# Performance work log

Measured on AMD Instinct MI355X. Metric: run time of the kernel, lower is better.

## Reference

```python
import jax, jax.numpy as jnp
import numpy as np

B, IN_F, K_INT, OUT_F = 256, 512, 75, 64
INIT = 0.05


def setup_inputs() -> dict:
    key = jax.random.key(0)
    k_x, k_t = jax.random.split(key)
    x = jax.random.normal(k_x, (B, IN_F), dtype=jnp.float32)
    T = jax.random.normal(k_t, (IN_F, K_INT, OUT_F), dtype=jnp.float32) * INIT
    return {"x": x, "T": T}


def reference(x, T):
    # M: [B, K, O] = x @ T flattened over (K, O)
    Bn = x.shape[0]
    M = (x @ T.reshape(T.shape[0], -1)).reshape(Bn, T.shape[1], T.shape[2])
    # pairwise L1 distance over K: [B, B, O]
    # (original materializes [B, B, K, O] broadcasted diff; same math)
    M_diff = M[None, :, :, :] - M[:, None, :, :]
    distance = jnp.abs(M_diff).sum(axis=2)           # [B, B, O]
    exp_distance = jnp.exp(-distance)                # [B, B, O]
    minibatch_features = exp_distance.sum(axis=1) - 1.0  # [B, O]; -1 removes self-distance
    return minibatch_features
```

## Files before the change

kernel.cpp:

```cpp
#include <hip/hip_runtime.h>


typedef __attribute__((ext_vector_type(8))) short bf16x8;
typedef __attribute__((ext_vector_type(4))) float f32x4;
typedef unsigned short u16;
typedef unsigned int u32;

__device__ inline u16 f2bf(float f) {
  u32 u = __float_as_uint(f);
  return (u16)((u + 0x7FFFu + ((u >> 16) & 1u)) >> 16);
}
__device__ inline short bftrunc(float f) {
  return (short)(__float_as_uint(f) >> 16);
}
__device__ inline float bflo(u32 u) { return __uint_as_float(u << 16); }
__device__ inline float bfhi(u32 u) { return __uint_as_float(u & 0xFFFF0000u); }

__global__ __launch_bounds__(256) void md_gemm_direct(const float* __restrict__ x,
                                                      const float* __restrict__ T,
                                                      float* __restrict__ Mt2) {
  const int tid = threadIdx.x;
  const int l = tid & 63, w = tid >> 6;
  const int bx = blockIdx.x;
  const int b0 = (blockIdx.y << 6) + ((w & 1) << 5);
  const int z = blockIdx.z;
  const int lr = l & 15;
  const int ko = (l >> 4) << 3;
  const int oh = (w >> 1) << 5;

  const float* At = T + (z * 256 + ko) * 4800 + bx * 64 + oh + lr;
  const float* Bx0 = x + (b0 + lr) * 512 + z * 256 + ko;
  const float* Bx1 = Bx0 + 16 * 512;

  f32x4 d00 = {0.f, 0.f, 0.f, 0.f}, d01 = d00, d10 = d00, d11 = d00;

#pragma unroll 2
  for (int kk = 0; kk < 8; ++kk) {
    bf16x8 a0, a1, f0, f1;
    const float* Ak = At + (kk << 5) * 4800;
#pragma unroll
    for (int e = 0; e < 8; ++e) {
      a0[e] = bftrunc(Ak[e * 4800]);
      a1[e] = bftrunc(Ak[e * 4800 + 16]);
    }
    const float4 b00 = *reinterpret_cast<const float4*>(Bx0 + (kk << 5));
    const float4 b01 = *reinterpret_cast<const float4*>(Bx0 + (kk << 5) + 4);
    const float4 b10 = *reinterpret_cast<const float4*>(Bx1 + (kk << 5));
    const float4 b11 = *reinterpret_cast<const float4*>(Bx1 + (kk << 5) + 4);
    f0[0] = bftrunc(b00.x); f0[1] = bftrunc(b00.y); f0[2] = bftrunc(b00.z); f0[3] = bftrunc(b00.w);
    f0[4] = bftrunc(b01.x); f0[5] = bftrunc(b01.y); f0[6] = bftrunc(b01.z); f0[7] = bftrunc(b01.w);
    f1[0] = bftrunc(b10.x); f1[1] = bftrunc(b10.y); f1[2] = bftrunc(b10.z); f1[3] = bftrunc(b10.w);
    f1[4] = bftrunc(b11.x); f1[5] = bftrunc(b11.y); f1[6] = bftrunc(b11.z); f1[7] = bftrunc(b11.w);

    d00 = __builtin_amdgcn_mfma_f32_16x16x32_bf16(a0, f0, d00, 0, 0, 0);
    d01 = __builtin_amdgcn_mfma_f32_16x16x32_bf16(a0, f1, d01, 0, 0, 0);
    d10 = __builtin_amdgcn_mfma_f32_16x16x32_bf16(a1, f0, d10, 0, 0, 0);
    d11 = __builtin_amdgcn_mfma_f32_16x16x32_bf16(a1, f1, d11, 0, 0, 0);
  }

  float* Mt = Mt2 + z * 1228800;
  const int n0 = (bx << 6) + oh;
#pragma unroll
  for (int r = 0; r < 4; ++r) {
    const int row = ((l >> 4) << 2) + r;
    {
      const int n = n0 + row;
      float* base = Mt + (n & 63) * 19200 + (n >> 6) * 256;
      base[b0 + lr] = d00[r];
      base[b0 + 16 + lr] = d01[r];
    }
    {
      const int n = n0 + 16 + row;
      float* base = Mt + (n & 63) * 19200 + (n >> 6) * 256;
      base[b0 + lr] = d10[r];
      base[b0 + 16 + lr] = d11[r];
    }
  }
}

#define PSTR 72
__global__ __launch_bounds__(256) void md_pair_sym(const float* __restrict__ Mt2,
                                                   float* __restrict__ out) {
  const int bid = blockIdx.x;
  const int o = bid & 63;
  const int tp = bid >> 6;
  const int TI[10] = {0, 0, 0, 0, 1, 1, 1, 2, 2, 3};
  const int TJ[10] = {0, 1, 2, 3, 1, 2, 3, 2, 3, 3};
  const int ti = TI[tp], tj = TJ[tp];
  const bool diag = (ti == tj);
  const int tid = threadIdx.x;

  __shared__ alignas(16) u16 panel[2][75 * PSTR];
  u16* Mi = panel[0];
  u16* Mj = diag ? panel[0] : panel[1];

  const float* M0 = Mt2 + o * 19200;
  const float* M1 = M0 + 1228800;

  for (int idx = tid; idx < 1200; idx += 256) {
    const int kk = idx >> 4, q = idx & 15;
    {
      const int goff = kk * 256 + (ti << 6) + (q << 2);
      const float4 v0 = *reinterpret_cast<const float4*>(M0 + goff);
      const float4 v1 = *reinterpret_cast<const float4*>(M1 + goff);
      uint2 p;
      p.x = (u32)f2bf(v0.x + v1.x) | ((u32)f2bf(v0.y + v1.y) << 16);
      p.y = (u32)f2bf(v0.z + v1.z) | ((u32)f2bf(v0.w + v1.w) << 16);
      *reinterpret_cast<uint2*>(Mi + kk * PSTR + (q << 2)) = p;
    }
    if (!diag) {
      const int goff = kk * 256 + (tj << 6) + (q << 2);
      const float4 v0 = *reinterpret_cast<const float4*>(M0 + goff);
      const float4 v1 = *reinterpret_cast<const float4*>(M1 + goff);
      uint2 p;
      p.x = (u32)f2bf(v0.x + v1.x) | ((u32)f2bf(v0.y + v1.y) << 16);
      p.y = (u32)f2bf(v0.z + v1.z) | ((u32)f2bf(v0.w + v1.w) << 16);
      *reinterpret_cast<uint2*>(Mj + kk * PSTR + (q << 2)) = p;
    }
  }
  __syncthreads();

  const int is = tid & 31;
  const int jg = tid >> 5;

  float d[2][8];
#pragma unroll
  for (int a = 0; a < 2; ++a)
#pragma unroll
    for (int b = 0; b < 8; ++b) d[a][b] = 0.0f;

#pragma unroll 15
  for (int kk = 0; kk < 75; ++kk) {
    const u32 vi = *reinterpret_cast<const u32*>(Mi + kk * PSTR + (is << 1));
    const uint4 ju = *reinterpret_cast<const uint4*>(Mj + kk * PSTR + (jg << 3));
    const float i0 = bflo(vi), i1 = bfhi(vi);
    const float ja[8] = {bflo(ju.x), bfhi(ju.x), bflo(ju.y), bfhi(ju.y),
                         bflo(ju.z), bfhi(ju.z), bflo(ju.w), bfhi(ju.w)};
#pragma unroll
    for (int b = 0; b < 8; ++b) {
      d[0][b] += __builtin_fabsf(ja[b] - i0);
      d[1][b] += __builtin_fabsf(ja[b] - i1);
    }
  }

  float isum[2] = {0.0f, 0.0f};
  float jsum[8] = {0.f, 0.f, 0.f, 0.f, 0.f, 0.f, 0.f, 0.f};
#pragma unroll
  for (int a = 0; a < 2; ++a) {
    const int gi = (ti << 6) + (is << 1) + a;
#pragma unroll
    for (int b = 0; b < 8; ++b) {
      const int gj = (tj << 6) + (jg << 3) + b;
      const float e = __expf(-d[a][b]);
      if (gi != gj) { isum[a] += e; jsum[b] += e; }
    }
  }

  __syncthreads();
  float* red = reinterpret_cast<float*>(panel);
  red[((is << 1) + 0) * 33 + jg] = isum[0];
  red[((is << 1) + 1) * 33 + jg] = isum[1];
  __syncthreads();
  if (tid < 64) {
    float t = 0.0f;
#pragma unroll
    for (int g = 0; g < 8; ++g) t += red[tid * 33 + g];
    atomicAdd(&out[((ti << 6) + tid) * 64 + o], t);
  }

  if (!diag) {
    __syncthreads();
#pragma unroll
    for (int b = 0; b < 8; ++b) red[((jg << 3) + b) * 33 + is] = jsum[b];
    __syncthreads();
    if (tid < 64) {
      float t = 0.0f;
#pragma unroll
      for (int g = 0; g < 32; ++g) t += red[tid * 33 + g];
      atomicAdd(&out[((tj << 6) + tid) * 64 + o], t);
    }
  }
}

extern "C" void kernel_launch(void* const* d_in, const int* in_sizes, int n_in,
                              void* d_out, int out_size, void* d_ws, size_t ws_size,
                              hipStream_t stream) {
  const float* x = (const float*)d_in[0];
  const float* T = (const float*)d_in[1];
  float* out = (float*)d_out;

  float* Mt2 = (float*)d_ws;

  hipMemsetAsync(out, 0, 256 * 64 * sizeof(float), stream);
  md_gemm_direct<<<dim3(75, 4, 2), 256, 0, stream>>>(x, T, Mt2);
  md_pair_sym<<<640, 256, 0, stream>>>(Mt2, out);
}
```

Before: 50.15 us.

## Split pairwise tile into half i-rows to double block count

The pairwise L1 kernel now splits each 64x64 tile pair into two 32-row halves along i, launching 1280 blocks instead of 640, so each thread handles one i row against eight j values. The i panel is stored as fp32 in shared memory while the j panel stays bf16. This is meant to raise occupancy and parallelism across CUs. In exchange the j panel is loaded and converted twice per tile, and the number of atomics on the j side doubles. The diagonal tiles now also load both panels separately.

```diff
diff --git a/kernel.cpp b/kernel.cpp
--- a/kernel.cpp
+++ b/kernel.cpp
@@ -78,105 +78,92 @@
   }
 }
 
-#define PSTR 72
-__global__ __launch_bounds__(256) void md_pair_sym(const float* __restrict__ Mt2,
-                                                   float* __restrict__ out) {
+#define JSTR 72
+#define ISTR 36
+__global__ __launch_bounds__(256) void md_pair_sym2(const float* __restrict__ Mt2,
+                                                    float* __restrict__ out) {
   const int bid = blockIdx.x;
   const int o = bid & 63;
-  const int tp = bid >> 6;
+  const int p = bid >> 6;
+  const int tp = p >> 1, h = p & 1;
   const int TI[10] = {0, 0, 0, 0, 1, 1, 1, 2, 2, 3};
   const int TJ[10] = {0, 1, 2, 3, 1, 2, 3, 2, 3, 3};
   const int ti = TI[tp], tj = TJ[tp];
   const bool diag = (ti == tj);
+  const int irow0 = (ti << 6) + (h << 5);
   const int tid = threadIdx.x;
 
-  __shared__ alignas(16) u16 panel[2][75 * PSTR];
-  u16* Mi = panel[0];
-  u16* Mj = diag ? panel[0] : panel[1];
+  __shared__ alignas(16) u16 Pj[75 * JSTR];
+  __shared__ alignas(16) float Pi[75 * ISTR];
 
   const float* M0 = Mt2 + o * 19200;
   const float* M1 = M0 + 1228800;
 
   for (int idx = tid; idx < 1200; idx += 256) {
     const int kk = idx >> 4, q = idx & 15;
-    {
-      const int goff = kk * 256 + (ti << 6) + (q << 2);
-      const float4 v0 = *reinterpret_cast<const float4*>(M0 + goff);
-      const float4 v1 = *reinterpret_cast<const float4*>(M1 + goff);
-      uint2 p;
-      p.x = (u32)f2bf(v0.x + v1.x) | ((u32)f2bf(v0.y + v1.y) << 16);
-      p.y = (u32)f2bf(v0.z + v1.z) | ((u32)f2bf(v0.w + v1.w) << 16);
-      *reinterpret_cast<uint2*>(Mi + kk * PSTR + (q << 2)) = p;
-    }
-    if (!diag) {
-      const int goff = kk * 256 + (tj << 6) + (q << 2);
-      const float4 v0 = *reinterpret_cast<const float4*>(M0 + goff);
-      const float4 v1 = *reinterpret_cast<const float4*>(M1 + goff);
-      uint2 p;
-      p.x = (u32)f2bf(v0.x + v1.x) | ((u32)f2bf(v0.y + v1.y) << 16);
-      p.y = (u32)f2bf(v0.z + v1.z) | ((u32)f2bf(v0.w + v1.w) << 16);
-      *reinterpret_cast<uint2*>(Mj + kk * PSTR + (q << 2)) = p;
-    }
+    const int goff = kk * 256 + (tj << 6) + (q << 2);
+    const float4 v0 = *reinterpret_cast<const float4*>(M0 + goff);
+    const float4 v1 = *reinterpret_cast<const float4*>(M1 + goff);
+    uint2 pk;
+    pk.x = (u32)f2bf(v0.x + v1.x) | ((u32)f2bf(v0.y + v1.y) << 16);
+    pk.y = (u32)f2bf(v0.z + v1.z) | ((u32)f2bf(v0.w + v1.w) << 16);
+    *reinterpret_cast<uint2*>(Pj + kk * JSTR + (q << 2)) = pk;
+  }
+  for (int idx = tid; idx < 2400; idx += 256) {
+    const int kk = idx >> 5, ii = idx & 31;
+    const int goff = kk * 256 + irow0 + ii;
+    Pi[kk * ISTR + ii] = M0[goff] + M1[goff];
   }
   __syncthreads();
 
-  const int is = tid & 31;
+  const int il = tid & 31;
   const int jg = tid >> 5;
 
-  float d[2][8];
+  float d[8];
 #pragma unroll
-  for (int a = 0; a < 2; ++a)
-#pragma unroll
-    for (int b = 0; b < 8; ++b) d[a][b] = 0.0f;
+  for (int b = 0; b < 8; ++b) d[b] = 0.0f;
 
 #pragma unroll 15
   for (int kk = 0; kk < 75; ++kk) {
-    const u32 vi = *reinterpret_cast<const u32*>(Mi + kk * PSTR + (is << 1));
-    const uint4 ju = *reinterpret_cast<const uint4*>(Mj + kk * PSTR + (jg << 3));
-    const float i0 = bflo(vi), i1 = bfhi(vi);
+    const float vi = Pi[kk * ISTR + il];
+    const uint4 ju = *reinterpret_cast<const uint4*>(Pj + kk * JSTR + (jg << 3));
     const float ja[8] = {bflo(ju.x), bfhi(ju.x), bflo(ju.y), bfhi(ju.y),
                          bflo(ju.z), bfhi(ju.z), bflo(ju.w), bfhi(ju.w)};
 #pragma unroll
-    for (int b = 0; b < 8; ++b) {
-      d[0][b] += __builtin_fabsf(ja[b] - i0);
-      d[1][b] += __builtin_fabsf(ja[b] - i1);
-    }
+    for (int b = 0; b < 8; ++b) d[b] += __builtin_fabsf(ja[b] - vi);
   }
 
-  float isum[2] = {0.0f, 0.0f};
+  float isum = 0.0f;
   float jsum[8] = {0.f, 0.f, 0.f, 0.f, 0.f, 0.f, 0.f, 0.f};
+  const int gi = irow0 + il;
 #pragma unroll
-  for (int a = 0; a < 2; ++a) {
-    const int gi = (ti << 6) + (is << 1) + a;
-#pragma unroll
-    for (int b = 0; b < 8; ++b) {
-      const int gj = (tj << 6) + (jg << 3) + b;
-      const float e = __expf(-d[a][b]);
-      if (gi != gj) { isum[a] += e; jsum[b] += e; }
-    }
+  for (int b = 0; b < 8; ++b) {
+    const int gj = (tj << 6) + (jg << 3) + b;
+    const float e = __expf(-d[b]);
+    if (gi != gj) { isum += e; jsum[b] += e; }
   }
 
   __syncthreads();
-  float* red = reinterpret_cast<float*>(panel);
-  red[((is << 1) + 0) * 33 + jg] = isum[0];
-  red[((is << 1) + 1) * 33 + jg] = isum[1];
+  float* red = reinterpret_cast<float*>(Pj);
+  red[il * 9 + jg] = isum;
   __syncthreads();
-  if (tid < 64) {
+  if (tid < 32) {
     float t = 0.0f;
 #pragma unroll
-    for (int g = 0; g < 8; ++g) t += red[tid * 33 + g];
-    atomicAdd(&out[((ti << 6) + tid) * 64 + o], t);
+    for (int g = 0; g < 8; ++g) t += red[tid * 9 + g];
+    atomicAdd(&out[(irow0 + tid) * 64 + o], t);
   }
 
   if (!diag) {
     __syncthreads();
+    float* red2 = reinterpret_cast<float*>(Pi);
 #pragma unroll
-    for (int b = 0; b < 8; ++b) red[((jg << 3) + b) * 33 + is] = jsum[b];
+    for (int b = 0; b < 8; ++b) red2[((jg << 3) + b) * 33 + il] = jsum[b];
     __syncthreads();
     if (tid < 64) {
       float t = 0.0f;
 #pragma unroll
-      for (int g = 0; g < 32; ++g) t += red[tid * 33 + g];
+      for (int g = 0; g < 32; ++g) t += red2[tid * 33 + g];
       atomicAdd(&out[((tj << 6) + tid) * 64 + o], t);
     }
   }
@@ -193,5 +180,5 @@
 
   hipMemsetAsync(out, 0, 256 * 64 * sizeof(float), stream);
   md_gemm_direct<<<dim3(75, 4, 2), 256, 0, stream>>>(x, T, Mt2);
-  md_pair_sym<<<640, 256, 0, stream>>>(Mt2, out);
+  md_pair_sym2<<<1280, 256, 0, stream>>>(Mt2, out);
 }
```

Result: no change. 49.60 us (median of 2 runs) (-1.1%).
